# Performance work log

Hardware: AMD Instinct MI355X
Metric: run time of the kernel (lower is better)

The kernel has to match this reference:

```python
import jax, jax.numpy as jnp
import numpy as np

N_MESH = 40962
N_GRID = 100000
N_EDGES = 400000
D_IN = 256
D_HID = 256
D_OUT = 128


def setup_inputs() -> dict:
    key = jax.random.key(0)
    k1, k2, k3, k4, k5 = jax.random.split(key, 5)
    mesh_features = jax.random.normal(k1, (N_MESH, D_IN), dtype=jnp.float32)
    src = jax.random.randint(k2, (N_EDGES,), 0, N_MESH)   # mesh node per edge
    dst = jax.random.randint(k3, (N_EDGES,), 0, N_GRID)   # grid node per edge
    edge_index = jnp.stack([src, dst], axis=0).astype(jnp.int64)
    # MLP params (Linear(D_IN,D_HID) -> SiLU -> Linear(D_HID,D_OUT))
    W1 = jax.random.normal(k4, (D_IN, D_HID), dtype=jnp.float32) / np.sqrt(D_IN)
    b1 = jnp.zeros((D_HID,), dtype=jnp.float32)
    W2 = jax.random.normal(k5, (D_HID, D_OUT), dtype=jnp.float32) / np.sqrt(D_HID)
    b2 = jnp.zeros((D_OUT,), dtype=jnp.float32)
    return {"mesh_features": mesh_features, "W1": W1, "b1": b1,
            "W2": W2, "b2": b2, "edge_index": edge_index,
            "n_grid_nodes": N_GRID}


def reference(mesh_features, W1, b1, W2, b2, edge_index, n_grid_nodes):
    # Gather mesh features along edges: (E, D_IN)
    msg = mesh_features[edge_index[0]]
    # Scatter-mean onto grid nodes
    sums = jax.ops.segment_sum(msg, edge_index[1], num_segments=n_grid_nodes)
    ones = jnp.ones((edge_index.shape[1],), dtype=mesh_features.dtype)
    cnt = jax.ops.segment_sum(ones, edge_index[1], num_segments=n_grid_nodes)
    grid_agg = sums / jnp.maximum(cnt, 1.0)[:, None]   # (N_grid, D_IN)
    # 2-layer MLP with SiLU
    h = jax.nn.silu(grid_agg @ W1 + b1)
    return h @ W2 + b2
```

## Files before the change

kernel.cpp:

```cpp
#include <hip/hip_runtime.h>
#include <cstdint>
#include <cstddef>


typedef _Float16 half8 __attribute__((ext_vector_type(8)));
typedef float floatx4 __attribute__((ext_vector_type(4)));

__global__ __launch_bounds__(256)
void prep_kernel(const float* __restrict__ W1, const float* __restrict__ W2,
                 _Float16* __restrict__ W1t, _Float16* __restrict__ W2t,
                 int* __restrict__ cnt, int NG) {
  int bid = (int)blockIdx.x;
  if (bid >= 96) {
    int idx = (bid - 96) * 1024 + (int)threadIdx.x * 4;
    if (idx + 3 < NG) *reinterpret_cast<int4*>(cnt + idx) = make_int4(0, 0, 0, 0);
    else { for (int k = 0; k < 4; ++k) if (idx + k < NG) cnt[idx + k] = 0; }
    return;
  }
  __shared__ float s[32][33];
  const float* src; _Float16* dst; int C, bx, by;
  if (bid < 64) { src = W1; dst = W1t; C = 256; bx = bid & 7; by = bid >> 3; }
  else { int id = bid - 64; src = W2; dst = W2t; C = 128; bx = id & 3; by = id >> 2; }
  const int R = 256;
  int tx = (int)(threadIdx.x & 31);
  int ty = (int)(threadIdx.x >> 5);
  int c0 = bx * 32, r0 = by * 32;
#pragma unroll
  for (int j = 0; j < 32; j += 8)
    s[ty + j][tx] = src[(size_t)(r0 + ty + j) * C + c0 + tx];
  __syncthreads();
#pragma unroll
  for (int j = 0; j < 32; j += 8)
    dst[(size_t)(c0 + ty + j) * R + r0 + tx] = (_Float16)s[tx][ty + j];
}

__global__ __launch_bounds__(256)
void gemm1_place_kernel(const float* __restrict__ A, const _Float16* __restrict__ Bt,
                        _Float16* __restrict__ outh, int M, int nG1,
                        const int* __restrict__ ei, int* __restrict__ cnt,
                        unsigned short* __restrict__ slots, int E) {
  const int bid = (int)blockIdx.x;
  const int tid = (int)threadIdx.x;
  __shared__ _Float16 ldsB[64 * 264];

  if (bid >= nG1) {
    int base = (bid - nG1) * 512;
    int e0 = base + tid;
    int e1 = base + 256 + tid;
    bool v0 = e0 < E, v1 = e1 < E;
    int s0 = 0, d0 = 0, s1 = 0, d1 = 0;
    if (v0) { s0 = ei[e0]; d0 = ei[E + e0]; }
    if (v1) { s1 = ei[e1]; d1 = ei[E + e1]; }
    if (v0) { int p = atomicAdd(&cnt[d0], 1);
              if (p < 32) slots[(size_t)d0 * 32 + p] = (unsigned short)s0; }
    if (v1) { int p = atomicAdd(&cnt[d1], 1);
              if (p < 32) slots[(size_t)d1 * 32 + p] = (unsigned short)s1; }
    return;
  }

  const int wid = tid >> 6;
  const int lane = tid & 63;
  const int r = lane & 15;
  const int kg = lane >> 4;
  const int mw = bid * 128 + wid * 32;

  int row0 = mw + r;       if (row0 > M - 1) row0 = M - 1;
  int row1 = mw + 16 + r;  if (row1 > M - 1) row1 = M - 1;
  const float* af0 = A + (size_t)row0 * 256 + kg * 8;
  const float* af1 = A + (size_t)row1 * 256 + kg * 8;

  half8 areg[2][8];
#pragma unroll
  for (int kk = 0; kk < 8; ++kk) {
    float4 f0 = *reinterpret_cast<const float4*>(af0 + kk * 32);
    float4 f1 = *reinterpret_cast<const float4*>(af0 + kk * 32 + 4);
    float4 g0 = *reinterpret_cast<const float4*>(af1 + kk * 32);
    float4 g1 = *reinterpret_cast<const float4*>(af1 + kk * 32 + 4);
    areg[0][kk] = (half8){(_Float16)f0.x, (_Float16)f0.y, (_Float16)f0.z, (_Float16)f0.w,
                          (_Float16)f1.x, (_Float16)f1.y, (_Float16)f1.z, (_Float16)f1.w};
    areg[1][kk] = (half8){(_Float16)g0.x, (_Float16)g0.y, (_Float16)g0.z, (_Float16)g0.w,
                          (_Float16)g1.x, (_Float16)g1.y, (_Float16)g1.z, (_Float16)g1.w};
  }

  for (int cq = 0; cq < 4; ++cq) {
    const int c0 = cq * 64;
    for (int i = tid; i < 64 * 32; i += 256) {
      int col = i >> 5;
      int ch = i & 31;
      *reinterpret_cast<half8*>(&ldsB[col * 264 + ch * 8]) =
          *reinterpret_cast<const half8*>(&Bt[(size_t)(c0 + col) * 256 + ch * 8]);
    }
    __syncthreads();

    floatx4 acc[2][4];
#pragma unroll
    for (int s = 0; s < 2; ++s)
#pragma unroll
      for (int j = 0; j < 4; ++j) acc[s][j] = (floatx4){0.f, 0.f, 0.f, 0.f};

#pragma unroll
    for (int kk = 0; kk < 8; ++kk) {
#pragma unroll
      for (int j = 0; j < 4; ++j) {
        half8 b = *reinterpret_cast<const half8*>(&ldsB[(j * 16 + r) * 264 + kk * 32 + kg * 8]);
        acc[0][j] = __builtin_amdgcn_mfma_f32_16x16x32_f16(areg[0][kk], b, acc[0][j], 0, 0, 0);
        acc[1][j] = __builtin_amdgcn_mfma_f32_16x16x32_f16(areg[1][kk], b, acc[1][j], 0, 0, 0);
      }
    }

    const int crow = kg * 4;
#pragma unroll
    for (int s = 0; s < 2; ++s) {
#pragma unroll
      for (int j = 0; j < 4; ++j) {
        int n = c0 + j * 16 + r;
#pragma unroll
        for (int i = 0; i < 4; ++i) {
          int m = mw + s * 16 + crow + i;
          if (m < M) outh[(size_t)m * 256 + n] = (_Float16)acc[s][j][i];
        }
      }
    }
    __syncthreads();
  }
}

__global__ __launch_bounds__(256)
void aggregate_kernel(const _Float16* __restrict__ mW1, const int* __restrict__ cnt,
                      const unsigned short* __restrict__ slots,
                      const float* __restrict__ b1, _Float16* __restrict__ h, int NG) {
  int wave = (int)((blockIdx.x * 256u + threadIdx.x) >> 6);
  int lane = (int)(threadIdx.x & 63);
  int half = lane >> 5;
  int l32 = lane & 31;
  int gA = wave * 4 + half * 2;
  int gB = gA + 1;
  bool vA = gA < NG, vB = gB < NG;
  int ga = vA ? gA : NG - 1;
  int gb = vB ? gB : NG - 1;

  int dA = cnt[ga]; if (dA > 32) dA = 32;
  int dB = cnt[gb]; if (dB > 32) dB = 32;
  int sA = (int)slots[(size_t)ga * 32 + l32];
  int sB = (int)slots[(size_t)gb * 32 + l32];
  const int sl0 = half * 32;

  float accA[8], accB[8];
#pragma unroll
  for (int k = 0; k < 8; ++k) { accA[k] = 0.f; accB[k] = 0.f; }

  int kmax = dA > dB ? dA : dB;
  for (int k = 0; k < kmax; k += 4) {
    int ia0 = __shfl(sA, sl0 + k + 0, 64);
    int ia1 = __shfl(sA, sl0 + k + 1, 64);
    int ia2 = __shfl(sA, sl0 + k + 2, 64);
    int ia3 = __shfl(sA, sl0 + k + 3, 64);
    int ib0 = __shfl(sB, sl0 + k + 0, 64);
    int ib1 = __shfl(sB, sl0 + k + 1, 64);
    int ib2 = __shfl(sB, sl0 + k + 2, 64);
    int ib3 = __shfl(sB, sl0 + k + 3, 64);
    if (k + 0 >= dA) ia0 = 0;  if (k + 1 >= dA) ia1 = 0;
    if (k + 2 >= dA) ia2 = 0;  if (k + 3 >= dA) ia3 = 0;
    if (k + 0 >= dB) ib0 = 0;  if (k + 1 >= dB) ib1 = 0;
    if (k + 2 >= dB) ib2 = 0;  if (k + 3 >= dB) ib3 = 0;
    half8 va0 = *reinterpret_cast<const half8*>(mW1 + (size_t)ia0 * 256 + l32 * 8);
    half8 va1 = *reinterpret_cast<const half8*>(mW1 + (size_t)ia1 * 256 + l32 * 8);
    half8 va2 = *reinterpret_cast<const half8*>(mW1 + (size_t)ia2 * 256 + l32 * 8);
    half8 va3 = *reinterpret_cast<const half8*>(mW1 + (size_t)ia3 * 256 + l32 * 8);
    half8 vb0 = *reinterpret_cast<const half8*>(mW1 + (size_t)ib0 * 256 + l32 * 8);
    half8 vb1 = *reinterpret_cast<const half8*>(mW1 + (size_t)ib1 * 256 + l32 * 8);
    half8 vb2 = *reinterpret_cast<const half8*>(mW1 + (size_t)ib2 * 256 + l32 * 8);
    half8 vb3 = *reinterpret_cast<const half8*>(mW1 + (size_t)ib3 * 256 + l32 * 8);
    float a0 = (k + 0 < dA) ? 1.f : 0.f;
    float a1 = (k + 1 < dA) ? 1.f : 0.f;
    float a2 = (k + 2 < dA) ? 1.f : 0.f;
    float a3 = (k + 3 < dA) ? 1.f : 0.f;
    float b0 = (k + 0 < dB) ? 1.f : 0.f;
    float b1s = (k + 1 < dB) ? 1.f : 0.f;
    float b2s = (k + 2 < dB) ? 1.f : 0.f;
    float b3 = (k + 3 < dB) ? 1.f : 0.f;
#pragma unroll
    for (int k8 = 0; k8 < 8; ++k8) {
      accA[k8] = fmaf((float)va0[k8], a0, accA[k8]);
      accA[k8] = fmaf((float)va1[k8], a1, accA[k8]);
      accA[k8] = fmaf((float)va2[k8], a2, accA[k8]);
      accA[k8] = fmaf((float)va3[k8], a3, accA[k8]);
      accB[k8] = fmaf((float)vb0[k8], b0, accB[k8]);
      accB[k8] = fmaf((float)vb1[k8], b1s, accB[k8]);
      accB[k8] = fmaf((float)vb2[k8], b2s, accB[k8]);
      accB[k8] = fmaf((float)vb3[k8], b3, accB[k8]);
    }
  }

  float rcA = __builtin_amdgcn_rcpf(fmaxf((float)dA, 1.0f));
  float rcB = __builtin_amdgcn_rcpf(fmaxf((float)dB, 1.0f));
  float4 blo = *reinterpret_cast<const float4*>(b1 + l32 * 8);
  float4 bhi = *reinterpret_cast<const float4*>(b1 + l32 * 8 + 4);
  float bb[8] = {blo.x, blo.y, blo.z, blo.w, bhi.x, bhi.y, bhi.z, bhi.w};
  half8 oA, oB;
#pragma unroll
  for (int k = 0; k < 8; ++k) {
    float xA = fmaf(accA[k], rcA, bb[k]);
    xA = xA * __builtin_amdgcn_rcpf(1.0f + __expf(-xA));
    oA[k] = (_Float16)xA;
    float xB = fmaf(accB[k], rcB, bb[k]);
    xB = xB * __builtin_amdgcn_rcpf(1.0f + __expf(-xB));
    oB[k] = (_Float16)xB;
  }
  if (vA) *reinterpret_cast<half8*>(h + (size_t)ga * 256 + l32 * 8) = oA;
  if (vB) *reinterpret_cast<half8*>(h + (size_t)gb * 256 + l32 * 8) = oB;
}

__global__ __launch_bounds__(512)
void mfma_gemm2(const _Float16* __restrict__ A, const _Float16* __restrict__ Bt,
                const float* __restrict__ bias, float* __restrict__ outf, int M) {
  __shared__ _Float16 ldsB[128 * 264];
  const int tid = (int)threadIdx.x;

  for (int i = tid; i < 128 * 32; i += 512) {
    int col = i >> 5;
    int ch = i & 31;
    *reinterpret_cast<half8*>(&ldsB[col * 264 + ch * 8]) =
        *reinterpret_cast<const half8*>(&Bt[(size_t)col * 256 + ch * 8]);
  }
  __syncthreads();

  const int wid = tid >> 6;
  const int lane = tid & 63;
  const int r = lane & 15;
  const int kg = lane >> 4;
  const int mw = (int)blockIdx.x * 256 + wid * 32;

  int row0 = mw + r;       if (row0 > M - 1) row0 = M - 1;
  int row1 = mw + 16 + r;  if (row1 > M - 1) row1 = M - 1;
  const _Float16* ah0 = A + (size_t)row0 * 256 + kg * 8;
  const _Float16* ah1 = A + (size_t)row1 * 256 + kg * 8;

  floatx4 acc[2][8];
#pragma unroll
  for (int s = 0; s < 2; ++s)
#pragma unroll
    for (int j = 0; j < 8; ++j) acc[s][j] = (floatx4){0.f, 0.f, 0.f, 0.f};

#pragma unroll
  for (int k0 = 0; k0 < 256; k0 += 32) {
    half8 a0 = *reinterpret_cast<const half8*>(ah0 + k0);
    half8 a1 = *reinterpret_cast<const half8*>(ah1 + k0);
#pragma unroll
    for (int j = 0; j < 8; ++j) {
      half8 b = *reinterpret_cast<const half8*>(&ldsB[(j * 16 + r) * 264 + k0 + kg * 8]);
      acc[0][j] = __builtin_amdgcn_mfma_f32_16x16x32_f16(a0, b, acc[0][j], 0, 0, 0);
      acc[1][j] = __builtin_amdgcn_mfma_f32_16x16x32_f16(a1, b, acc[1][j], 0, 0, 0);
    }
  }

  const int crow = kg * 4;
#pragma unroll
  for (int s = 0; s < 2; ++s) {
#pragma unroll
    for (int j = 0; j < 8; ++j) {
      int n = j * 16 + r;
      float bv = bias[n];
#pragma unroll
      for (int i = 0; i < 4; ++i) {
        int m = mw + s * 16 + crow + i;
        if (m < M) outf[(size_t)m * 128 + n] = acc[s][j][i] + bv;
      }
    }
  }
}

extern "C" void kernel_launch(void* const* d_in, const int* in_sizes, int n_in,
                              void* d_out, int out_size, void* d_ws, size_t ws_size,
                              hipStream_t stream) {
  const float* mesh = (const float*)d_in[0];
  const float* W1   = (const float*)d_in[1];
  const float* b1   = (const float*)d_in[2];
  const float* W2   = (const float*)d_in[3];
  const float* b2   = (const float*)d_in[4];
  const int*   ei   = (const int*)d_in[5];

  const int NM = in_sizes[0] / 256;
  const int E  = in_sizes[5] / 2;
  const int NG = out_size / 128;

  char* w = (char*)d_ws;
  _Float16* meshW1 = (_Float16*)w;                 w += (size_t)NM * 256 * 2;
  _Float16* h      = (_Float16*)w;                 w += (size_t)NG * 256 * 2;
  _Float16* W1t    = (_Float16*)w;                 w += 256 * 256 * 2;
  _Float16* W2t    = (_Float16*)w;                 w += 128 * 256 * 2;
  int* cnt = (int*)w;                              w += (size_t)NG * 4;
  unsigned short* slots = (unsigned short*)w;      w += (size_t)NG * 32 * 2;

  int zblk = (NG + 1023) / 1024;
  prep_kernel<<<96 + zblk, 256, 0, stream>>>(W1, W2, W1t, W2t, cnt, NG);

  int nG1 = (NM + 127) / 128;
  int nPl = (E + 511) / 512;
  gemm1_place_kernel<<<nG1 + nPl, 256, 0, stream>>>(
      mesh, W1t, meshW1, NM, nG1, ei, cnt, slots, E);

  aggregate_kernel<<<(NG + 15) / 16, 256, 0, stream>>>(meshW1, cnt, slots, b1, h, NG);

  mfma_gemm2<<<(NG + 255) / 256, 512, 0, stream>>>(h, W2t, b2, (float*)d_out, NG);
}
```

Before: 94.34 us.

## Fuse aggregation+SiLU with second GEMM via per-wave LDS tile

Merges the aggregate kernel and the second MFMA GEMM into one kernel. Each wave aggregates 16 grid nodes into an LDS tile of h and then multiplies it by W2t with MFMA, writing the output directly. This removes the global write and re-read of the fp16 hidden matrix and one kernel launch. In exchange, W2t is read from global/L2 by every wave rather than staged in LDS, and there is less parallelism per node group, since each wave now handles four sequential aggregation iterations.

```diff
diff --git a/kernel.cpp b/kernel.cpp
--- a/kernel.cpp
+++ b/kernel.cpp
@@ -126,146 +126,118 @@
 }
 
 __global__ __launch_bounds__(256)
-void aggregate_kernel(const _Float16* __restrict__ mW1, const int* __restrict__ cnt,
+void agg_gemm2_kernel(const _Float16* __restrict__ mW1, const int* __restrict__ cnt,
                       const unsigned short* __restrict__ slots,
-                      const float* __restrict__ b1, _Float16* __restrict__ h, int NG) {
-  int wave = (int)((blockIdx.x * 256u + threadIdx.x) >> 6);
-  int lane = (int)(threadIdx.x & 63);
-  int half = lane >> 5;
-  int l32 = lane & 31;
-  int gA = wave * 4 + half * 2;
-  int gB = gA + 1;
-  bool vA = gA < NG, vB = gB < NG;
-  int ga = vA ? gA : NG - 1;
-  int gb = vB ? gB : NG - 1;
-
-  int dA = cnt[ga]; if (dA > 32) dA = 32;
-  int dB = cnt[gb]; if (dB > 32) dB = 32;
-  int sA = (int)slots[(size_t)ga * 32 + l32];
-  int sB = (int)slots[(size_t)gb * 32 + l32];
-  const int sl0 = half * 32;
-
-  float accA[8], accB[8];
-#pragma unroll
-  for (int k = 0; k < 8; ++k) { accA[k] = 0.f; accB[k] = 0.f; }
-
-  int kmax = dA > dB ? dA : dB;
-  for (int k = 0; k < kmax; k += 4) {
-    int ia0 = __shfl(sA, sl0 + k + 0, 64);
-    int ia1 = __shfl(sA, sl0 + k + 1, 64);
-    int ia2 = __shfl(sA, sl0 + k + 2, 64);
-    int ia3 = __shfl(sA, sl0 + k + 3, 64);
-    int ib0 = __shfl(sB, sl0 + k + 0, 64);
-    int ib1 = __shfl(sB, sl0 + k + 1, 64);
-    int ib2 = __shfl(sB, sl0 + k + 2, 64);
-    int ib3 = __shfl(sB, sl0 + k + 3, 64);
-    if (k + 0 >= dA) ia0 = 0;  if (k + 1 >= dA) ia1 = 0;
-    if (k + 2 >= dA) ia2 = 0;  if (k + 3 >= dA) ia3 = 0;
-    if (k + 0 >= dB) ib0 = 0;  if (k + 1 >= dB) ib1 = 0;
-    if (k + 2 >= dB) ib2 = 0;  if (k + 3 >= dB) ib3 = 0;
-    half8 va0 = *reinterpret_cast<const half8*>(mW1 + (size_t)ia0 * 256 + l32 * 8);
-    half8 va1 = *reinterpret_cast<const half8*>(mW1 + (size_t)ia1 * 256 + l32 * 8);
-    half8 va2 = *reinterpret_cast<const half8*>(mW1 + (size_t)ia2 * 256 + l32 * 8);
-    half8 va3 = *reinterpret_cast<const half8*>(mW1 + (size_t)ia3 * 256 + l32 * 8);
-    half8 vb0 = *reinterpret_cast<const half8*>(mW1 + (size_t)ib0 * 256 + l32 * 8);
-    half8 vb1 = *reinterpret_cast<const half8*>(mW1 + (size_t)ib1 * 256 + l32 * 8);
-    half8 vb2 = *reinterpret_cast<const half8*>(mW1 + (size_t)ib2 * 256 + l32 * 8);
-    half8 vb3 = *reinterpret_cast<const half8*>(mW1 + (size_t)ib3 * 256 + l32 * 8);
-    float a0 = (k + 0 < dA) ? 1.f : 0.f;
-    float a1 = (k + 1 < dA) ? 1.f : 0.f;
-    float a2 = (k + 2 < dA) ? 1.f : 0.f;
-    float a3 = (k + 3 < dA) ? 1.f : 0.f;
-    float b0 = (k + 0 < dB) ? 1.f : 0.f;
-    float b1s = (k + 1 < dB) ? 1.f : 0.f;
-    float b2s = (k + 2 < dB) ? 1.f : 0.f;
-    float b3 = (k + 3 < dB) ? 1.f : 0.f;
-#pragma unroll
-    for (int k8 = 0; k8 < 8; ++k8) {
-      accA[k8] = fmaf((float)va0[k8], a0, accA[k8]);
-      accA[k8] = fmaf((float)va1[k8], a1, accA[k8]);
-      accA[k8] = fmaf((float)va2[k8], a2, accA[k8]);
-      accA[k8] = fmaf((float)va3[k8], a3, accA[k8]);
-      accB[k8] = fmaf((float)vb0[k8], b0, accB[k8]);
-      accB[k8] = fmaf((float)vb1[k8], b1s, accB[k8]);
-      accB[k8] = fmaf((float)vb2[k8], b2s, accB[k8]);
-      accB[k8] = fmaf((float)vb3[k8], b3, accB[k8]);
-    }
-  }
-
-  float rcA = __builtin_amdgcn_rcpf(fmaxf((float)dA, 1.0f));
-  float rcB = __builtin_amdgcn_rcpf(fmaxf((float)dB, 1.0f));
+                      const float* __restrict__ b1, const _Float16* __restrict__ W2t,
+                      const float* __restrict__ b2, float* __restrict__ out, int NG) {
+  __shared__ _Float16 hT[4][16 * 268];
+  const int tid = (int)threadIdx.x;
+  const int wid = tid >> 6;
+  const int lane = tid & 63;
+  const int half = lane >> 5;
+  const int l32 = lane & 31;
+  const int nb = ((int)blockIdx.x * 4 + wid) * 16;
+  _Float16* hw = &hT[wid][0];
+
   float4 blo = *reinterpret_cast<const float4*>(b1 + l32 * 8);
   float4 bhi = *reinterpret_cast<const float4*>(b1 + l32 * 8 + 4);
   float bb[8] = {blo.x, blo.y, blo.z, blo.w, bhi.x, bhi.y, bhi.z, bhi.w};
-  half8 oA, oB;
-#pragma unroll
-  for (int k = 0; k < 8; ++k) {
-    float xA = fmaf(accA[k], rcA, bb[k]);
-    xA = xA * __builtin_amdgcn_rcpf(1.0f + __expf(-xA));
-    oA[k] = (_Float16)xA;
-    float xB = fmaf(accB[k], rcB, bb[k]);
-    xB = xB * __builtin_amdgcn_rcpf(1.0f + __expf(-xB));
-    oB[k] = (_Float16)xB;
-  }
-  if (vA) *reinterpret_cast<half8*>(h + (size_t)ga * 256 + l32 * 8) = oA;
-  if (vB) *reinterpret_cast<half8*>(h + (size_t)gb * 256 + l32 * 8) = oB;
-}
-
-__global__ __launch_bounds__(512)
-void mfma_gemm2(const _Float16* __restrict__ A, const _Float16* __restrict__ Bt,
-                const float* __restrict__ bias, float* __restrict__ outf, int M) {
-  __shared__ _Float16 ldsB[128 * 264];
-  const int tid = (int)threadIdx.x;
-
-  for (int i = tid; i < 128 * 32; i += 512) {
-    int col = i >> 5;
-    int ch = i & 31;
-    *reinterpret_cast<half8*>(&ldsB[col * 264 + ch * 8]) =
-        *reinterpret_cast<const half8*>(&Bt[(size_t)col * 256 + ch * 8]);
-  }
-  __syncthreads();
-
-  const int wid = tid >> 6;
-  const int lane = tid & 63;
+
+  for (int it = 0; it < 4; ++it) {
+    int gA = nb + it * 4 + half * 2;
+    int gB = gA + 1;
+    int ga = gA < NG ? gA : NG - 1;
+    int gb = gB < NG ? gB : NG - 1;
+
+    int dA = cnt[ga]; if (dA > 32) dA = 32;
+    int dB = cnt[gb]; if (dB > 32) dB = 32;
+    int sA = (int)slots[(size_t)ga * 32 + l32];
+    int sB = (int)slots[(size_t)gb * 32 + l32];
+    const int sl0 = half * 32;
+
+    float accA[8], accB[8];
+#pragma unroll
+    for (int k = 0; k < 8; ++k) { accA[k] = 0.f; accB[k] = 0.f; }
+
+    int kmax = dA > dB ? dA : dB;
+    for (int k = 0; k < kmax; k += 4) {
+      int ia0 = __shfl(sA, sl0 + k + 0, 64);
+      int ia1 = __shfl(sA, sl0 + k + 1, 64);
+      int ia2 = __shfl(sA, sl0 + k + 2, 64);
+      int ia3 = __shfl(sA, sl0 + k + 3, 64);
+      int ib0 = __shfl(sB, sl0 + k + 0, 64);
+      int ib1 = __shfl(sB, sl0 + k + 1, 64);
+      int ib2 = __shfl(sB, sl0 + k + 2, 64);
+      int ib3 = __shfl(sB, sl0 + k + 3, 64);
+      if (k + 0 >= dA) ia0 = 0;  if (k + 1 >= dA) ia1 = 0;
+      if (k + 2 >= dA) ia2 = 0;  if (k + 3 >= dA) ia3 = 0;
+      if (k + 0 >= dB) ib0 = 0;  if (k + 1 >= dB) ib1 = 0;
+      if (k + 2 >= dB) ib2 = 0;  if (k + 3 >= dB) ib3 = 0;
+      half8 va0 = *reinterpret_cast<const half8*>(mW1 + (size_t)ia0 * 256 + l32 * 8);
+      half8 va1 = *reinterpret_cast<const half8*>(mW1 + (size_t)ia1 * 256 + l32 * 8);
+      half8 va2 = *reinterpret_cast<const half8*>(mW1 + (size_t)ia2 * 256 + l32 * 8);
+      half8 va3 = *reinterpret_cast<const half8*>(mW1 + (size_t)ia3 * 256 + l32 * 8);
+      half8 vb0 = *reinterpret_cast<const half8*>(mW1 + (size_t)ib0 * 256 + l32 * 8);
+      half8 vb1 = *reinterpret_cast<const half8*>(mW1 + (size_t)ib1 * 256 + l32 * 8);
+      half8 vb2 = *reinterpret_cast<const half8*>(mW1 + (size_t)ib2 * 256 + l32 * 8);
+      half8 vb3 = *reinterpret_cast<const half8*>(mW1 + (size_t)ib3 * 256 + l32 * 8);
+      float a0 = (k + 0 < dA) ? 1.f : 0.f;
+      float a1 = (k + 1 < dA) ? 1.f : 0.f;
+      float a2 = (k + 2 < dA) ? 1.f : 0.f;
+      float a3 = (k + 3 < dA) ? 1.f : 0.f;
+      float b0 = (k + 0 < dB) ? 1.f : 0.f;
+      float b1s = (k + 1 < dB) ? 1.f : 0.f;
+      float b2s = (k + 2 < dB) ? 1.f : 0.f;
+      float b3 = (k + 3 < dB) ? 1.f : 0.f;
+#pragma unroll
+      for (int k8 = 0; k8 < 8; ++k8) {
+        accA[k8] = fmaf((float)va0[k8], a0, accA[k8]);
+        accA[k8] = fmaf((float)va1[k8], a1, accA[k8]);
+        accA[k8] = fmaf((float)va2[k8], a2, accA[k8]);
+        accA[k8] = fmaf((float)va3[k8], a3, accA[k8]);
+        accB[k8] = fmaf((float)vb0[k8], b0, accB[k8]);
+        accB[k8] = fmaf((float)vb1[k8], b1s, accB[k8]);
+        accB[k8] = fmaf((float)vb2[k8], b2s, accB[k8]);
+        accB[k8] = fmaf((float)vb3[k8], b3, accB[k8]);
+      }
+    }
+
+    float rcA = __builtin_amdgcn_rcpf(fmaxf((float)dA, 1.0f));
+    float rcB = __builtin_amdgcn_rcpf(fmaxf((float)dB, 1.0f));
+    half8 oA, oB;
+#pragma unroll
+    for (int k = 0; k < 8; ++k) {
+      float xA = fmaf(accA[k], rcA, bb[k]);
+      xA = xA * __builtin_amdgcn_rcpf(1.0f + __expf(-xA));
+      oA[k] = (_Float16)xA;
+      float xB = fmaf(accB[k], rcB, bb[k]);
+      xB = xB * __builtin_amdgcn_rcpf(1.0f + __expf(-xB));
+      oB[k] = (_Float16)xB;
+    }
+    *reinterpret_cast<half8*>(&hw[(it * 4 + half * 2 + 0) * 268 + l32 * 8]) = oA;
+    *reinterpret_cast<half8*>(&hw[(it * 4 + half * 2 + 1) * 268 + l32 * 8]) = oB;
+  }
+
   const int r = lane & 15;
   const int kg = lane >> 4;
-  const int mw = (int)blockIdx.x * 256 + wid * 32;
-
-  int row0 = mw + r;       if (row0 > M - 1) row0 = M - 1;
-  int row1 = mw + 16 + r;  if (row1 > M - 1) row1 = M - 1;
-  const _Float16* ah0 = A + (size_t)row0 * 256 + kg * 8;
-  const _Float16* ah1 = A + (size_t)row1 * 256 + kg * 8;
-
-  floatx4 acc[2][8];
-#pragma unroll
-  for (int s = 0; s < 2; ++s)
-#pragma unroll
-    for (int j = 0; j < 8; ++j) acc[s][j] = (floatx4){0.f, 0.f, 0.f, 0.f};
-
-#pragma unroll
-  for (int k0 = 0; k0 < 256; k0 += 32) {
-    half8 a0 = *reinterpret_cast<const half8*>(ah0 + k0);
-    half8 a1 = *reinterpret_cast<const half8*>(ah1 + k0);
-#pragma unroll
-    for (int j = 0; j < 8; ++j) {
-      half8 b = *reinterpret_cast<const half8*>(&ldsB[(j * 16 + r) * 264 + k0 + kg * 8]);
-      acc[0][j] = __builtin_amdgcn_mfma_f32_16x16x32_f16(a0, b, acc[0][j], 0, 0, 0);
-      acc[1][j] = __builtin_amdgcn_mfma_f32_16x16x32_f16(a1, b, acc[1][j], 0, 0, 0);
-    }
-  }
-
   const int crow = kg * 4;
-#pragma unroll
-  for (int s = 0; s < 2; ++s) {
-#pragma unroll
-    for (int j = 0; j < 8; ++j) {
-      int n = j * 16 + r;
-      float bv = bias[n];
-#pragma unroll
-      for (int i = 0; i < 4; ++i) {
-        int m = mw + s * 16 + crow + i;
-        if (m < M) outf[(size_t)m * 128 + n] = acc[s][j][i] + bv;
-      }
+
+#pragma unroll
+  for (int j = 0; j < 8; ++j) {
+    const _Float16* bp = W2t + (size_t)(j * 16 + r) * 256 + kg * 8;
+    floatx4 acc2 = (floatx4){0.f, 0.f, 0.f, 0.f};
+#pragma unroll
+    for (int k0 = 0; k0 < 256; k0 += 32) {
+      half8 a = *reinterpret_cast<const half8*>(&hw[r * 268 + k0 + kg * 8]);
+      half8 b = *reinterpret_cast<const half8*>(bp + k0);
+      acc2 = __builtin_amdgcn_mfma_f32_16x16x32_f16(a, b, acc2, 0, 0, 0);
+    }
+    int n = j * 16 + r;
+    float bv = b2[n];
+#pragma unroll
+    for (int i = 0; i < 4; ++i) {
+      int m = nb + crow + i;
+      if (m < NG) out[(size_t)m * 128 + n] = acc2[i] + bv;
     }
   }
 }
@@ -286,7 +258,6 @@
 
   char* w = (char*)d_ws;
   _Float16* meshW1 = (_Float16*)w;                 w += (size_t)NM * 256 * 2;
-  _Float16* h      = (_Float16*)w;                 w += (size_t)NG * 256 * 2;
   _Float16* W1t    = (_Float16*)w;                 w += 256 * 256 * 2;
   _Float16* W2t    = (_Float16*)w;                 w += 128 * 256 * 2;
   int* cnt = (int*)w;                              w += (size_t)NG * 4;
@@ -300,7 +271,6 @@
   gemm1_place_kernel<<<nG1 + nPl, 256, 0, stream>>>(
       mesh, W1t, meshW1, NM, nG1, ei, cnt, slots, E);
 
-  aggregate_kernel<<<(NG + 15) / 16, 256, 0, stream>>>(meshW1, cnt, slots, b1, h, NG);
-
-  mfma_gemm2<<<(NG + 255) / 256, 512, 0, stream>>>(h, W2t, b2, (float*)d_out, NG);
-}
+  agg_gemm2_kernel<<<(NG + 63) / 64, 256, 0, stream>>>(
+      meshW1, cnt, slots, b1, W2t, b2, (float*)d_out, NG);
+}
```

Result: slower. 118.2 us (+25.3%).
